# Kernel tuning notes

Measured on AMD Instinct MI355X. Metric: run time of the kernel, lower is better.

Reference implementation:

```python
import jax, jax.numpy as jnp
import numpy as np

C = 16          # in_channels // 4
EXP = 16        # expand_rate
SHIFTS = [1, 3, 5, 7]
BN_EPS = 1e-5

# fixed directional-difference kernels (non-trainable in the torch module)
_tmp1 = np.array([[[-1,0,0],[0,1,0],[0,0,0]],
                  [[0,-1,0],[0,1,0],[0,0,0]],
                  [[0,0,-1],[0,1,0],[0,0,0]],
                  [[0,0,0],[-1,1,0],[0,0,0]]], dtype=np.float32).reshape(4,1,3,3)
_tmp2 = _tmp1[:, :, ::-1, ::-1].copy()
K1 = jnp.asarray(np.tile(np.concatenate([_tmp1, _tmp2], 0), (C,1,1,1)))  # [8C,1,3,3]
K2 = jnp.asarray(np.tile(np.concatenate([_tmp2, _tmp1], 0), (C,1,1,1)))  # [8C,1,3,3]

def conv(x, w, groups=1, dilation=1, bias=None):
    out = jax.lax.conv_general_dilated(
        x, w, window_strides=(1,1), padding='SAME',
        rhs_dilation=(dilation, dilation),
        dimension_numbers=('NCHW','OIHW','NCHW'),
        feature_group_count=groups)
    if bias is not None:
        out = out + bias[None, :, None, None]
    return out

def setup_inputs() -> dict:
    key = jax.random.key(0)
    ks = jax.random.split(key, 20)
    B, Cin, H, W = 4, 64, 256, 256
    inp = {
        'cen': jax.random.normal(ks[0], (B, Cin, H, W), jnp.float32),
        'mas': jax.random.normal(ks[1], (B, 1, H, W), jnp.float32),
        'w_in': jax.random.normal(ks[2], (C, Cin, 1, 1), jnp.float32) * 0.1,
        'b_in': jax.random.normal(ks[3], (C,), jnp.float32) * 0.1,
        'w_c0': jax.random.normal(ks[4], (C, C, 1, 1), jnp.float32) * 0.1,
        'b_c0': jax.random.normal(ks[5], (C,), jnp.float32) * 0.1,
        'w_c1': jax.random.normal(ks[6], (C, C, 3, 3), jnp.float32) * 0.1,
        'b_c1': jax.random.normal(ks[7], (C,), jnp.float32) * 0.1,
        'w_c2': jax.random.normal(ks[8], (C, C, 5, 5), jnp.float32) * 0.05,
        'b_c2': jax.random.normal(ks[9], (C,), jnp.float32) * 0.1,
        'w_c3': jax.random.normal(ks[10], (C, C, 7, 7), jnp.float32) * 0.05,
        'b_c3': jax.random.normal(ks[11], (C,), jnp.float32) * 0.1,
        'scales1': jax.random.normal(ks[12], (4,), jnp.float32) * 0.1,
        'scales2': jax.random.normal(ks[13], (C * EXP, 8, 1, 1), jnp.float32) * 0.1,
        'scales3': jax.random.normal(ks[14], (C, EXP, 1, 1), jnp.float32) * 0.1,
        'w_base': jax.random.normal(ks[15], (C, C, 3, 3), jnp.float32) * 0.1,
        'bn_gamma': jnp.ones((C,), jnp.float32),
        'bn_beta': jnp.zeros((C,), jnp.float32),
        'bn_mean': jnp.zeros((C,), jnp.float32),
        'bn_var': jnp.ones((C,), jnp.float32),
        'w_out': jax.random.normal(ks[16], (1, C, 1, 1), jnp.float32) * 0.1,
        'b_out': jax.random.normal(ks[17], (1,), jnp.float32) * 0.1,
    }
    return inp

def reference(cen, mas, w_in, b_in, w_c0, b_c0, w_c1, b_c1, w_c2, b_c2, w_c3, b_c3,
              scales1, scales2, scales3, w_base, bn_gamma, bn_beta, bn_mean, bn_var,
              w_out, b_out):
    x = conv(cen, w_in, bias=b_in)                      # [B,C,H,W]
    k3 = jax.nn.softmax(scales2, axis=1)                # [8C*2? no: [C*EXP,8,1,1]
    k4 = jax.nn.softmax(scales3, axis=1)                # [C,EXP,1,1]
    conv_ws = [(w_c0, b_c0), (w_c1, b_c1), (w_c2, b_c2), (w_c3, b_c3)]
    outs = []
    for (wc, bc), shift in zip(conv_ws, SHIFTS):
        c = conv(x, wc, bias=bc)                        # [B,C,H,W]
        o1 = conv(c, K1, groups=C, dilation=shift)      # [B,8C,H,W]
        o2 = conv(c, K2, groups=C, dilation=shift)
        o1 = conv(o1, k3, groups=C)                     # [B,C*EXP,H,W]
        o2 = conv(o2, k3, groups=C)
        o = jnp.sort(o1 * o2, axis=2)                   # sort along H
        o = jax.nn.silu(o)
        o = conv(o, k4, groups=C)                       # [B,C,H,W]
        outs.append(o)
    outs = jnp.stack(outs, axis=-1)                     # [B,C,H,W,4]
    outs = jnp.max(outs, axis=-1) + jnp.mean(outs, axis=-1)
    # out_conv = BaseConv(3x3 conv -> BN(eval) -> SiLU) then 1x1 conv to 1 ch
    h = conv(outs, w_base)
    h = (h - bn_mean[None, :, None, None]) * jax.lax.rsqrt(bn_var + BN_EPS)[None, :, None, None]
    h = h * bn_gamma[None, :, None, None] + bn_beta[None, :, None, None]
    h = jax.nn.silu(h)
    h = conv(h, w_out, bias=b_out)
    out_mask = jax.nn.sigmoid(h)                        # [B,1,H,W]
    s = jax.nn.softmax(scales1, axis=-1)
    m = jax.nn.sigmoid(mas)
    return cen * (out_mask * m * s[0] + m * s[1] + s[2] * out_mask + s[3])
```

## Files before the change

### kernel.cpp

```cpp
#include <hip/hip_runtime.h>

#define HW 65536

constexpr int OFF_X    = 0;
constexpr int OFF_CT   = 4194304;
constexpr int OFF_MAX  = 8388608;
constexpr int OFF_SUM  = 12582912;
constexpr int P_K3  = 17039360;
constexpr int P_K3S = P_K3  + 2048;
constexpr int P_K4  = P_K3S + 2048;
constexpr int P_S1  = P_K4  + 256;
constexpr int P_BNS = P_S1  + 4;
constexpr int P_BNB = P_BNS + 16;
constexpr int P_WRI = P_BNB + 16;
constexpr int P_WR0 = P_WRI + 1024;
constexpr int P_WR1 = P_WR0 + 256;
constexpr int P_WR2 = P_WR1 + 2304;
constexpr int P_WR3 = P_WR2 + 6400;
constexpr int P_WRB = P_WR3 + 12544;
constexpr int P_K3U = P_WRB + 2304;
constexpr int P_K3V = P_K3U + 512;

typedef _Float16 hv2 __attribute__((ext_vector_type(2)));

__device__ __forceinline__ int h2i(hv2 v) { return __builtin_bit_cast(int, v); }
__device__ __forceinline__ hv2 i2h(int v) { return __builtin_bit_cast(hv2, v); }

__device__ __forceinline__ hv2 pkrtz(float a, float b) {
  return __builtin_bit_cast(hv2, __builtin_amdgcn_cvt_pkrtz(a, b));
}

__device__ __forceinline__ hv2 pk_fma_n(hv2 a, hv2 b, hv2 c) {
#if __has_builtin(__builtin_elementwise_fma)
  return __builtin_elementwise_fma(a, b, c);
#else
  return a * b + c;
#endif
}

__device__ __forceinline__ hv2 pkmin(hv2 a, hv2 b) {
  hv2 d; asm("v_pk_min_f16 %0, %1, %2" : "=v"(d) : "v"(a), "v"(b)); return d;
}
__device__ __forceinline__ hv2 pkmax(hv2 a, hv2 b) {
  hv2 d; asm("v_pk_max_f16 %0, %1, %2" : "=v"(d) : "v"(a), "v"(b)); return d;
}
__device__ __forceinline__ hv2 pkmul(hv2 a, hv2 b) {
  hv2 d; asm("v_pk_mul_f16 %0, %1, %2" : "=v"(d) : "v"(a), "v"(b)); return d;
}
__device__ __forceinline__ hv2 pkfma(hv2 a, hv2 b, hv2 c) {
  hv2 d; asm("v_pk_fma_f16 %0, %1, %2, %3" : "=v"(d) : "v"(a), "v"(b), "v"(c)); return d;
}

__device__ __forceinline__ hv2 sel32(bool c, hv2 a, hv2 b) {
  return i2h(c ? h2i(a) : h2i(b));
}

template <int LMASK>
__device__ __forceinline__ int lane_xor_i(int x) {
  if constexpr (LMASK < 32) {
    return __builtin_amdgcn_ds_swizzle(x, (LMASK << 10) | 0x1F);
  } else {
    return __shfl_xor(x, LMASK, 64);
  }
}

__device__ __forceinline__ float sigmoid_fast(float x) {
  return __fdividef(1.0f, 1.0f + __expf(-x));
}

__global__ void k_prep(const float* __restrict__ w_in, const float* __restrict__ w_c0,
                       const float* __restrict__ w_c1, const float* __restrict__ w_c2,
                       const float* __restrict__ w_c3, const float* __restrict__ w_base,
                       const float* __restrict__ scales1, const float* __restrict__ scales2,
                       const float* __restrict__ scales3, const float* __restrict__ bn_gamma,
                       const float* __restrict__ bn_beta, const float* __restrict__ bn_mean,
                       const float* __restrict__ bn_var, float* __restrict__ ws) {
  int tid = threadIdx.x;
  {
    const float* srow = scales2 + tid * 8;
    float v[8]; float mx = -1e30f;
    for (int j = 0; j < 8; j++) { v[j] = srow[j]; mx = fmaxf(mx, v[j]); }
    float s = 0.f;
    for (int j = 0; j < 8; j++) { v[j] = __expf(v[j] - mx); s += v[j]; }
    float inv = 1.0f / s;
    for (int j = 0; j < 8; j++) ws[P_K3 + tid * 8 + j] = v[j] * inv;
  }
  if (tid < 16) {
    const float* srow = scales3 + tid * 16;
    float v[16]; float mx = -1e30f;
    for (int e = 0; e < 16; e++) { v[e] = srow[e]; mx = fmaxf(mx, v[e]); }
    float s = 0.f;
    for (int e = 0; e < 16; e++) { v[e] = __expf(v[e] - mx); s += v[e]; }
    float inv = 1.0f / s;
    for (int e = 0; e < 16; e++) ws[P_K4 + tid * 16 + e] = v[e] * inv;
  }
  if (tid == 0) {
    float v[4]; float mx = -1e30f;
    for (int i = 0; i < 4; i++) { v[i] = scales1[i]; mx = fmaxf(mx, v[i]); }
    float s = 0.f;
    for (int i = 0; i < 4; i++) { v[i] = __expf(v[i] - mx); s += v[i]; }
    for (int i = 0; i < 4; i++) ws[P_S1 + i] = v[i] / s;
  }
  if (tid < 16) {
    float rs = rsqrtf(bn_var[tid] + 1e-5f);
    float sc = bn_gamma[tid] * rs;
    ws[P_BNS + tid] = sc;
    ws[P_BNB + tid] = bn_beta[tid] - bn_mean[tid] * sc;
  }
  for (int i = tid; i < 1024; i += 256) { int ci = i >> 4, co = i & 15; ws[P_WRI + i] = w_in[co * 64 + ci]; }
  {
    uint32_t* w0 = (uint32_t*)(ws + P_WR0);
    for (int i = tid; i < 128; i += 256) {
      int cp = i & 7, ci = i >> 3;
      hv2 wv;
      wv.x = (_Float16)w_c0[(2 * cp) * 16 + ci];
      wv.y = (_Float16)w_c0[(2 * cp + 1) * 16 + ci];
      w0[ci * 8 + cp] = __builtin_bit_cast(uint32_t, wv);
    }
    uint32_t* w1 = (uint32_t*)(ws + P_WR1);
    for (int i = tid; i < 1152; i += 256) {
      int cp = i & 7; int r = i >> 3; int kw = r % 3; r /= 3; int kh = r % 3; int ci = r / 3;
      hv2 wv;
      wv.x = (_Float16)w_c1[((2 * cp) * 16 + ci) * 9 + kh * 3 + kw];
      wv.y = (_Float16)w_c1[((2 * cp + 1) * 16 + ci) * 9 + kh * 3 + kw];
      w1[((ci * 3 + kh) * 3 + kw) * 8 + cp] = __builtin_bit_cast(uint32_t, wv);
    }
    uint32_t* w2 = (uint32_t*)(ws + P_WR2);
    for (int i = tid; i < 3200; i += 256) {
      int cp = i & 7; int r = i >> 3; int kw = r % 5; r /= 5; int kh = r % 5; int ci = r / 5;
      hv2 wv;
      wv.x = (_Float16)w_c2[((2 * cp) * 16 + ci) * 25 + kh * 5 + kw];
      wv.y = (_Float16)w_c2[((2 * cp + 1) * 16 + ci) * 25 + kh * 5 + kw];
      w2[((ci * 5 + kh) * 5 + kw) * 8 + cp] = __builtin_bit_cast(uint32_t, wv);
    }
    uint32_t* w3 = (uint32_t*)(ws + P_WR3);
    for (int i = tid; i < 6272; i += 256) {
      int cp = i & 7; int r = i >> 3; int kw = r % 7; r /= 7; int kh = r % 7; int ci = r / 7;
      hv2 wv;
      wv.x = (_Float16)w_c3[((2 * cp) * 16 + ci) * 49 + kh * 7 + kw];
      wv.y = (_Float16)w_c3[((2 * cp + 1) * 16 + ci) * 49 + kh * 7 + kw];
      w3[((ci * 7 + kh) * 7 + kw) * 8 + cp] = __builtin_bit_cast(uint32_t, wv);
    }
  }
  for (int i = tid; i < 2304; i += 256) {
    int co = i & 15; int r = i >> 4; int kh = r % 3; r /= 3; int kw = r % 3; int g = r / 3;
    ws[P_WRB + i] = w_base[((co * 16 + g) * 3 + kh) * 3 + kw];
  }
  __syncthreads();
  uint32_t* k3u = (uint32_t*)(ws + P_K3U);
  uint32_t* k3v = (uint32_t*)(ws + P_K3V);
  for (int i = tid; i < 512; i += 256) {
    int g = i >> 5, p = (i >> 2) & 7, j = i & 3;
    const float* r0 = ws + P_K3 + g * 128 + (2 * p) * 8;
    const float* r1 = ws + P_K3 + g * 128 + (2 * p + 1) * 8;
    hv2 wu, wv;
    wu.x = (_Float16)((r0[j] + r0[j + 4]) * 0.5f);
    wu.y = (_Float16)((r1[j] + r1[j + 4]) * 0.5f);
    wv.x = (_Float16)((r0[j] - r0[j + 4]) * 0.5f);
    wv.y = (_Float16)((r1[j] - r1[j + 4]) * 0.5f);
    k3u[i] = __builtin_bit_cast(uint32_t, wu);
    k3v[i] = __builtin_bit_cast(uint32_t, wv);
  }
}

__global__ __launch_bounds__(256) void k_in(const float* __restrict__ cen,
                                            const float* __restrict__ b_in,
                                            const float* __restrict__ ws,
                                            float* __restrict__ xT) {
  __shared__ float ldst[16 * 16 * 17];
  int tid = threadIdx.x;
  int b = blockIdx.z;
  int hbase = blockIdx.y * 16, wbase = blockIdx.x * 16;
  int ty = tid >> 4, tx = tid & 15;
  const float* wri = ws + P_WRI;
  float acc[16];
#pragma unroll
  for (int co = 0; co < 16; co++) acc[co] = b_in[co];
  const float* cp = cen + b * 64 * HW + (hbase + ty) * 256 + wbase + tx;
#pragma unroll 4
  for (int ci = 0; ci < 64; ci++) {
    float v = cp[ci * HW];
#pragma unroll
    for (int co = 0; co < 16; co++) acc[co] = fmaf(wri[ci * 16 + co], v, acc[co]);
  }
#pragma unroll
  for (int co = 0; co < 16; co++) ldst[(co * 16 + tx) * 17 + ty] = acc[co];
  __syncthreads();
  int wy = tid >> 4, hx = tid & 15;
#pragma unroll
  for (int ci = 0; ci < 16; ci++) {
    xT[((b * 16 + ci) << 16) + (wbase + wy) * 256 + hbase + hx] =
        ldst[(ci * 16 + wy) * 17 + hx];
  }
}

template <int KS, bool SAFE>
__device__ __forceinline__ void conv_body(const float* __restrict__ xb,
                                          const uint32_t* __restrict__ wrh,
                                          int w, int hbase, int lane, hv2 acc[8]) {
  constexpr int P = KS / 2;
#pragma unroll 2
  for (int ci = 0; ci < 16; ci++) {
#pragma unroll
    for (int kw = 0; kw < KS; kw++) {
      const int wc = w + kw - P;
      if (KS > 1 && (unsigned)wc >= 256u) continue;
      const float* col = xb + (ci << 16) + (wc << 8);
      const int hb = hbase + lane - P;
#pragma unroll
      for (int kh = 0; kh < KS; kh++) {
        float tv;
        if constexpr (SAFE) {
          tv = col[hb + kh];
        } else {
          const int h = hb + kh;
          tv = ((unsigned)h < 256u) ? col[h] : 0.0f;
        }
        const hv2 tp = pkrtz(tv, tv);
        const uint32_t* wp = wrh + ((ci * KS + kh) * KS + kw) * 8;
#pragma unroll
        for (int cp = 0; cp < 8; cp++)
          acc[cp] = pk_fma_n(i2h((int)wp[cp]), tp, acc[cp]);
      }
    }
  }
}

template <int KS>
__global__ __launch_bounds__(256) void k_conv(const float* __restrict__ xT,
                                              const float* __restrict__ bias,
                                              const uint32_t* __restrict__ wrh,
                                              float* __restrict__ cT) {
  const int tid = threadIdx.x;
  const int lane = tid & 63;
  const int wv = (blockIdx.x << 2) + (tid >> 6);
  const int hseg = wv & 3;
  const int w = (wv >> 2) & 255;
  const int b = wv >> 10;
  const int hbase = hseg << 6;
  const float* xb = xT + ((b * 16) << 16);

  hv2 acc[8];
#pragma unroll
  for (int cp = 0; cp < 8; cp++) {
    hv2 bv;
    bv.x = (_Float16)bias[2 * cp];
    bv.y = (_Float16)bias[2 * cp + 1];
    acc[cp] = bv;
  }

  if (KS == 1 || (hseg != 0 && hseg != 3)) {
    conv_body<KS, true>(xb, wrh, w, hbase, lane, acc);
  } else {
    conv_body<KS, false>(xb, wrh, w, hbase, lane, acc);
  }

  float* o = cT + ((b * 16) << 16) + (w << 8) + hbase + lane;
#pragma unroll
  for (int cp = 0; cp < 8; cp++) {
    o[(2 * cp) << 16] = (float)acc[cp].x;
    o[(2 * cp + 1) << 16] = (float)acc[cp].y;
  }
}

__device__ __forceinline__ void ce_pair_h(hv2& a, hv2& b, bool up) {
  hv2 lo = pkmin(a, b);
  hv2 hi = pkmax(a, b);
  a = sel32(up, lo, hi);
  b = sel32(up, hi, lo);
}

template <int SIZE, int DIST>
__device__ __forceinline__ void stage_x_h(hv2 v[4], int i0) {
  const bool keepmin = (((i0 & DIST) == 0) == ((i0 & SIZE) == 0));
#pragma unroll
  for (int r = 0; r < 4; r++) {
    hv2 pv = i2h(lane_xor_i<(DIST >> 2)>(h2i(v[r])));
    v[r] = sel32(keepmin, pkmin(v[r], pv), pkmax(v[r], pv));
  }
}

template <int SIZE>
__device__ __forceinline__ void stage_d21_h(hv2 v[4], int i0) {
  bool up = ((i0 & SIZE) == 0);
  ce_pair_h(v[0], v[2], up); ce_pair_h(v[1], v[3], up);
  ce_pair_h(v[0], v[1], up); ce_pair_h(v[2], v[3], up);
}

__device__ __forceinline__ void sort256h(hv2 v[4], int lane) {
  int i0 = lane << 2;
  ce_pair_h(v[0], v[1], true); ce_pair_h(v[2], v[3], false);
  stage_d21_h<4>(v, i0);
  stage_x_h<8, 4>(v, i0); stage_d21_h<8>(v, i0);
  stage_x_h<16, 8>(v, i0); stage_x_h<16, 4>(v, i0); stage_d21_h<16>(v, i0);
  stage_x_h<32, 16>(v, i0); stage_x_h<32, 8>(v, i0); stage_x_h<32, 4>(v, i0); stage_d21_h<32>(v, i0);
  stage_x_h<64, 32>(v, i0); stage_x_h<64, 16>(v, i0); stage_x_h<64, 8>(v, i0); stage_x_h<64, 4>(v, i0); stage_d21_h<64>(v, i0);
  stage_x_h<128, 64>(v, i0); stage_x_h<128, 32>(v, i0); stage_x_h<128, 16>(v, i0); stage_x_h<128, 8>(v, i0); stage_x_h<128, 4>(v, i0); stage_d21_h<128>(v, i0);
  stage_x_h<256, 128>(v, i0); stage_x_h<256, 64>(v, i0); stage_x_h<256, 32>(v, i0); stage_x_h<256, 16>(v, i0); stage_x_h<256, 8>(v, i0); stage_x_h<256, 4>(v, i0); stage_d21_h<256>(v, i0);
}

template <int DIL>
__global__ __launch_bounds__(256) void k_branch(const float* __restrict__ cT,
                                                const float* __restrict__ ws,
                                                float* __restrict__ maxb,
                                                float* __restrict__ sumb,
                                                int initFlag) {
  const int tid = threadIdx.x;
  const int lane = tid & 63;
  const int wid = __builtin_amdgcn_readfirstlane(tid >> 6);
  const int wv = (blockIdx.x << 2) + wid;
  const int w = wv & 255;
  const int g = (wv >> 8) & 15;
  const int b = wv >> 12;
  const float* base = cT + ((b * 16 + g) << 16);

  float vals[3][3][4];
#pragma unroll
  for (int wi = 0; wi < 3; ++wi) {
    const int wc = w + (wi - 1) * DIL;
    const bool wok = ((unsigned)wc < 256u);
    const float* col = base + (wok ? wc : 0) * 256;
#pragma unroll
    for (int si = 0; si < 3; ++si) {
#pragma unroll
      for (int r = 0; r < 4; ++r) {
        const int h = lane + (r << 6) + (si - 1) * DIL;
        const bool ok = wok && ((unsigned)h < 256u);
        vals[wi][si][r] = ok ? col[h] : 0.0f;
      }
    }
  }
  hv2 uh[4][4], vh[4][4];
#pragma unroll
  for (int r = 0; r < 4; ++r) {
    const float c0 = vals[1][1][r];
    float d0 = c0 - vals[0][0][r];
    float d1 = c0 - vals[1][0][r];
    float d2 = c0 - vals[2][0][r];
    float d3 = c0 - vals[0][1][r];
    float d4 = c0 - vals[2][2][r];
    float d5 = c0 - vals[1][2][r];
    float d6 = c0 - vals[0][2][r];
    float d7 = c0 - vals[2][1][r];
    uh[0][r] = pkrtz(d0 + d4, d0 + d4);
    uh[1][r] = pkrtz(d1 + d5, d1 + d5);
    uh[2][r] = pkrtz(d2 + d6, d2 + d6);
    uh[3][r] = pkrtz(d3 + d7, d3 + d7);
    vh[0][r] = pkrtz(d0 - d4, d0 - d4);
    vh[1][r] = pkrtz(d1 - d5, d1 - d5);
    vh[2][r] = pkrtz(d2 - d6, d2 - d6);
    vh[3][r] = pkrtz(d3 - d7, d3 - d7);
  }
  float out[4] = {0.f, 0.f, 0.f, 0.f};
  const uint32_t* k3u = (const uint32_t*)(ws + P_K3U) + g * 32;
  const uint32_t* k3v = (const uint32_t*)(ws + P_K3V) + g * 32;
  const float* k4p = ws + P_K4 + g * 16;
#pragma unroll 1
  for (int p = 0; p < 8; ++p) {
    hv2 t[4];
    hv2 wu[4], wvv[4];
#pragma unroll
    for (int j = 0; j < 4; ++j) {
      wu[j]  = i2h((int)k3u[p * 4 + j]);
      wvv[j] = i2h((int)k3v[p * 4 + j]);
    }
#pragma unroll
    for (int r = 0; r < 4; ++r) {
      hv2 s = pkmul(wu[0], uh[0][r]);
      s = pkfma(wu[1], uh[1][r], s);
      s = pkfma(wu[2], uh[2][r], s);
      s = pkfma(wu[3], uh[3][r], s);
      hv2 d = pkmul(wvv[0], vh[0][r]);
      d = pkfma(wvv[1], vh[1][r], d);
      d = pkfma(wvv[2], vh[2][r], d);
      d = pkfma(wvv[3], vh[3][r], d);
      t[r] = pkmul(s + d, s - d);
    }
    sort256h(t, lane);
    const float k4a = k4p[2 * p], k4b = k4p[2 * p + 1];
#pragma unroll
    for (int r = 0; r < 4; ++r) {
      const float va = (float)t[r].x;
      const float vb = (float)t[r].y;
      out[r] = fmaf(k4a, va * sigmoid_fast(va), out[r]);
      out[r] = fmaf(k4b, vb * sigmoid_fast(vb), out[r]);
    }
  }
  const int obase = (((b * 16 + g) << 8) + w) * 256 + (lane << 2);
  float4 o4 = make_float4(out[0], out[1], out[2], out[3]);
  float4* mp = (float4*)(maxb + obase);
  float4* sp = (float4*)(sumb + obase);
  if (initFlag) {
    *mp = o4;
    *sp = o4;
  } else {
    float4 m = *mp;
    m.x = fmaxf(m.x, o4.x); m.y = fmaxf(m.y, o4.y);
    m.z = fmaxf(m.z, o4.z); m.w = fmaxf(m.w, o4.w);
    *mp = m;
    float4 s = *sp;
    s.x += o4.x; s.y += o4.y; s.z += o4.z; s.w += o4.w;
    *sp = s;
  }
}

__global__ __launch_bounds__(256) void k_tail(const float* __restrict__ maxb,
                                              const float* __restrict__ sumb,
                                              const float* __restrict__ ws,
                                              const float* __restrict__ cen,
                                              const float* __restrict__ mas,
                                              const float* __restrict__ w_out,
                                              const float* __restrict__ b_out,
                                              float* __restrict__ out) {
  __shared__ float lds[16 * 18 * 18];
  __shared__ float ldsf[256];
  int tid = threadIdx.x;
  int b = blockIdx.z;
  int wbase = blockIdx.x * 16, hbase = blockIdx.y * 16;
  const float* mb = maxb + (b * 16) * HW;
  const float* sb = sumb + (b * 16) * HW;
  for (int i = tid; i < 16 * 18 * 18; i += 256) {
    int g = i / 324; int r = i % 324; int xx = r / 18, yy = r % 18;
    int wq = wbase + xx - 1, hq = hbase + yy - 1;
    float v = 0.0f;
    if (wq >= 0 && wq < 256 && hq >= 0 && hq < 256) {
      int idx = g * HW + wq * 256 + hq;
      v = mb[idx] + 0.25f * sb[idx];
    }
    lds[i] = v;
  }
  __syncthreads();
  int xw = tid >> 4, yh = tid & 15;
  float acc[16] = {0.f, 0.f, 0.f, 0.f, 0.f, 0.f, 0.f, 0.f,
                   0.f, 0.f, 0.f, 0.f, 0.f, 0.f, 0.f, 0.f};
  for (int g = 0; g < 16; g++) {
#pragma unroll
    for (int kw = 0; kw < 3; kw++) {
#pragma unroll
      for (int kh = 0; kh < 3; kh++) {
        float v = lds[g * 324 + (xw + kw) * 18 + (yh + kh)];
        const float* wp = ws + P_WRB + ((g * 3 + kw) * 3 + kh) * 16;
#pragma unroll
        for (int co = 0; co < 16; co++) acc[co] = fmaf(wp[co], v, acc[co]);
      }
    }
  }
  float mo = b_out[0];
#pragma unroll
  for (int co = 0; co < 16; co++) {
    float z = acc[co] * ws[P_BNS + co] + ws[P_BNB + co];
    float sl = z * sigmoid_fast(z);
    mo = fmaf(w_out[co], sl, mo);
  }
  float mk = sigmoid_fast(mo);
  ldsf[yh * 16 + xw] = mk;
  __syncthreads();
  {
    int yy = tid >> 4, xx = tid & 15;
    float mkv = ldsf[yy * 16 + xx];
    float m = sigmoid_fast(mas[b * HW + (hbase + yy) * 256 + wbase + xx]);
    float s0 = ws[P_S1], s1 = ws[P_S1 + 1], s2 = ws[P_S1 + 2], s3 = ws[P_S1 + 3];
    float f = mkv * m * s0 + m * s1 + s2 * mkv + s3;
    ldsf[yy * 16 + xx] = f;
  }
  __syncthreads();
  const float* cb = cen + b * 64 * HW;
  float* ob = out + b * 64 * HW;
#pragma unroll 4
  for (int it = 0; it < 16; ++it) {
    int flat = it * 256 + tid;
    int ci = flat >> 6;
    int rr = flat & 63;
    int yy = rr >> 2, wq = rr & 3;
    const float* fr = &ldsf[yy * 16 + wq * 4];
    float4 f4 = make_float4(fr[0], fr[1], fr[2], fr[3]);
    int addr = ci * HW + (hbase + yy) * 256 + wbase + wq * 4;
    const float4 c4 = *(const float4*)(cb + addr);
    float4 o4;
    o4.x = c4.x * f4.x; o4.y = c4.y * f4.y; o4.z = c4.z * f4.z; o4.w = c4.w * f4.w;
    *(float4*)(ob + addr) = o4;
  }
}

extern "C" void kernel_launch(void* const* d_in, const int* in_sizes, int n_in,
                              void* d_out, int out_size, void* d_ws, size_t ws_size,
                              hipStream_t stream) {
  (void)in_sizes; (void)n_in; (void)out_size; (void)ws_size;
  const float* cen = (const float*)d_in[0];
  const float* mas = (const float*)d_in[1];
  const float* w_in = (const float*)d_in[2];
  const float* b_in = (const float*)d_in[3];
  const float* w_c0 = (const float*)d_in[4];
  const float* b_c0 = (const float*)d_in[5];
  const float* w_c1 = (const float*)d_in[6];
  const float* b_c1 = (const float*)d_in[7];
  const float* w_c2 = (const float*)d_in[8];
  const float* b_c2 = (const float*)d_in[9];
  const float* w_c3 = (const float*)d_in[10];
  const float* b_c3 = (const float*)d_in[11];
  const float* scales1 = (const float*)d_in[12];
  const float* scales2 = (const float*)d_in[13];
  const float* scales3 = (const float*)d_in[14];
  const float* w_base = (const float*)d_in[15];
  const float* bn_gamma = (const float*)d_in[16];
  const float* bn_beta = (const float*)d_in[17];
  const float* bn_mean = (const float*)d_in[18];
  const float* bn_var = (const float*)d_in[19];
  const float* w_out = (const float*)d_in[20];
  const float* b_out = (const float*)d_in[21];
  float* ws = (float*)d_ws;
  float* out = (float*)d_out;

  float* xT = ws + OFF_X;
  float* cT = ws + OFF_CT;
  float* maxb = ws + OFF_MAX;
  float* sumb = ws + OFF_SUM;

  k_prep<<<1, 256, 0, stream>>>(w_in, w_c0, w_c1, w_c2, w_c3, w_base, scales1, scales2,
                                scales3, bn_gamma, bn_beta, bn_mean, bn_var, ws);
  k_in<<<dim3(16, 16, 4), 256, 0, stream>>>(cen, b_in, ws, xT);

  k_conv<1><<<1024, 256, 0, stream>>>(xT, b_c0, (const uint32_t*)(ws + P_WR0), cT);
  k_branch<1><<<4096, 256, 0, stream>>>(cT, ws, maxb, sumb, 1);
  k_conv<3><<<1024, 256, 0, stream>>>(xT, b_c1, (const uint32_t*)(ws + P_WR1), cT);
  k_branch<3><<<4096, 256, 0, stream>>>(cT, ws, maxb, sumb, 0);
  k_conv<5><<<1024, 256, 0, stream>>>(xT, b_c2, (const uint32_t*)(ws + P_WR2), cT);
  k_branch<5><<<4096, 256, 0, stream>>>(cT, ws, maxb, sumb, 0);
  k_conv<7><<<1024, 256, 0, stream>>>(xT, b_c3, (const uint32_t*)(ws + P_WR3), cT);
  k_branch<7><<<4096, 256, 0, stream>>>(cT, ws, maxb, sumb, 0);

  k_tail<<<dim3(16, 16, 4), 256, 0, stream>>>(maxb, sumb, ws, cen, mas, w_out, b_out, out);
}
```

Before: 865.0 us.

## Fuse four dilation branches into one kernel with in-register max/mean reduction

Stores all four conv outputs in separate workspace slices, then runs a single branch kernel that processes every dilation per wave and reduces max plus 0.25·sum in registers. This writes one combined buffer instead of repeatedly reading and writing max and sum buffers, and cuts the launch count. The parameter region is moved to the front of the workspace, and a fallback path keeps the old per-branch sequence when the workspace is too small. The fused kernel does four times the work per wave, which lengthens its runtime and may raise register pressure.

```diff
diff --git a/kernel.cpp b/kernel.cpp
--- a/kernel.cpp
+++ b/kernel.cpp
@@ -2,24 +2,22 @@
 
 #define HW 65536
 
-constexpr int OFF_X    = 0;
-constexpr int OFF_CT   = 4194304;
-constexpr int OFF_MAX  = 8388608;
-constexpr int OFF_SUM  = 12582912;
-constexpr int P_K3  = 17039360;
-constexpr int P_K3S = P_K3  + 2048;
-constexpr int P_K4  = P_K3S + 2048;
-constexpr int P_S1  = P_K4  + 256;
-constexpr int P_BNS = P_S1  + 4;
-constexpr int P_BNB = P_BNS + 16;
-constexpr int P_WRI = P_BNB + 16;
-constexpr int P_WR0 = P_WRI + 1024;
-constexpr int P_WR1 = P_WR0 + 256;
-constexpr int P_WR2 = P_WR1 + 2304;
-constexpr int P_WR3 = P_WR2 + 6400;
-constexpr int P_WRB = P_WR3 + 12544;
-constexpr int P_K3U = P_WRB + 2304;
-constexpr int P_K3V = P_K3U + 512;
+constexpr int P_K3  = 0;
+constexpr int P_K4  = 2048;
+constexpr int P_S1  = 2304;
+constexpr int P_BNS = 2308;
+constexpr int P_BNB = 2324;
+constexpr int P_WRI = 2340;
+constexpr int P_WR0 = 3364;
+constexpr int P_WR1 = 3492;
+constexpr int P_WR2 = 4644;
+constexpr int P_WR3 = 7844;
+constexpr int P_WRB = 14116;
+constexpr int P_K3U = 16420;
+constexpr int P_K3V = 16932;
+constexpr int OFF_X  = 32768;
+constexpr int OFF_CT = 32768 + 4194304;
+constexpr int CTSZ   = 4194304;
 
 typedef _Float16 hv2 __attribute__((ext_vector_type(2)));
 
@@ -300,20 +298,9 @@
 }
 
 template <int DIL>
-__global__ __launch_bounds__(256) void k_branch(const float* __restrict__ cT,
-                                                const float* __restrict__ ws,
-                                                float* __restrict__ maxb,
-                                                float* __restrict__ sumb,
-                                                int initFlag) {
-  const int tid = threadIdx.x;
-  const int lane = tid & 63;
-  const int wid = __builtin_amdgcn_readfirstlane(tid >> 6);
-  const int wv = (blockIdx.x << 2) + wid;
-  const int w = wv & 255;
-  const int g = (wv >> 8) & 15;
-  const int b = wv >> 12;
-  const float* base = cT + ((b * 16 + g) << 16);
-
+__device__ __forceinline__ void branch_one(const float* __restrict__ base,
+                                           const float* __restrict__ ws,
+                                           int g, int w, int lane, float out[4]) {
   float vals[3][3][4];
 #pragma unroll
   for (int wi = 0; wi < 3; ++wi) {
@@ -351,7 +338,7 @@
     vh[2][r] = pkrtz(d2 - d6, d2 - d6);
     vh[3][r] = pkrtz(d3 - d7, d3 - d7);
   }
-  float out[4] = {0.f, 0.f, 0.f, 0.f};
+  out[0] = out[1] = out[2] = out[3] = 0.f;
   const uint32_t* k3u = (const uint32_t*)(ws + P_K3U) + g * 32;
   const uint32_t* k3v = (const uint32_t*)(ws + P_K3V) + g * 32;
   const float* k4p = ws + P_K4 + g * 16;
@@ -386,6 +373,60 @@
       out[r] = fmaf(k4b, vb * sigmoid_fast(vb), out[r]);
     }
   }
+}
+
+__global__ __launch_bounds__(256) void k_branch4(const float* __restrict__ cT,
+                                                 const float* __restrict__ ws,
+                                                 float* __restrict__ comb) {
+  const int tid = threadIdx.x;
+  const int lane = tid & 63;
+  const int wid = __builtin_amdgcn_readfirstlane(tid >> 6);
+  const int wv = (blockIdx.x << 2) + wid;
+  const int w = wv & 255;
+  const int g = (wv >> 8) & 15;
+  const int b = wv >> 12;
+  const int boff = (b * 16 + g) << 16;
+
+  float out[4], mx[4], sm[4];
+  branch_one<1>(cT + 0 * CTSZ + boff, ws, g, w, lane, out);
+#pragma unroll
+  for (int r = 0; r < 4; ++r) { mx[r] = out[r]; sm[r] = out[r]; }
+  branch_one<3>(cT + 1 * CTSZ + boff, ws, g, w, lane, out);
+#pragma unroll
+  for (int r = 0; r < 4; ++r) { mx[r] = fmaxf(mx[r], out[r]); sm[r] += out[r]; }
+  branch_one<5>(cT + 2 * CTSZ + boff, ws, g, w, lane, out);
+#pragma unroll
+  for (int r = 0; r < 4; ++r) { mx[r] = fmaxf(mx[r], out[r]); sm[r] += out[r]; }
+  branch_one<7>(cT + 3 * CTSZ + boff, ws, g, w, lane, out);
+#pragma unroll
+  for (int r = 0; r < 4; ++r) { mx[r] = fmaxf(mx[r], out[r]); sm[r] += out[r]; }
+
+  const int obase = (((b * 16 + g) << 8) + w) * 256 + (lane << 2);
+  float4 o4;
+  o4.x = fmaf(0.25f, sm[0], mx[0]);
+  o4.y = fmaf(0.25f, sm[1], mx[1]);
+  o4.z = fmaf(0.25f, sm[2], mx[2]);
+  o4.w = fmaf(0.25f, sm[3], mx[3]);
+  *(float4*)(comb + obase) = o4;
+}
+
+template <int DIL>
+__global__ __launch_bounds__(256) void k_branch(const float* __restrict__ cT,
+                                                const float* __restrict__ ws,
+                                                float* __restrict__ maxb,
+                                                float* __restrict__ sumb,
+                                                int initFlag) {
+  const int tid = threadIdx.x;
+  const int lane = tid & 63;
+  const int wid = __builtin_amdgcn_readfirstlane(tid >> 6);
+  const int wv = (blockIdx.x << 2) + wid;
+  const int w = wv & 255;
+  const int g = (wv >> 8) & 15;
+  const int b = wv >> 12;
+
+  float out[4];
+  branch_one<DIL>(cT + ((b * 16 + g) << 16), ws, g, w, lane, out);
+
   const int obase = (((b * 16 + g) << 8) + w) * 256 + (lane << 2);
   float4 o4 = make_float4(out[0], out[1], out[2], out[3]);
   float4* mp = (float4*)(maxb + obase);
@@ -404,28 +445,30 @@
   }
 }
 
-__global__ __launch_bounds__(256) void k_tail(const float* __restrict__ maxb,
-                                              const float* __restrict__ sumb,
+__global__ __launch_bounds__(256) void k_tail(const float* __restrict__ a,
+                                              const float* __restrict__ sb,
                                               const float* __restrict__ ws,
                                               const float* __restrict__ cen,
                                               const float* __restrict__ mas,
                                               const float* __restrict__ w_out,
                                               const float* __restrict__ b_out,
-                                              float* __restrict__ out) {
+                                              float* __restrict__ out,
+                                              int combMode) {
   __shared__ float lds[16 * 18 * 18];
   __shared__ float ldsf[256];
   int tid = threadIdx.x;
   int b = blockIdx.z;
   int wbase = blockIdx.x * 16, hbase = blockIdx.y * 16;
-  const float* mb = maxb + (b * 16) * HW;
-  const float* sb = sumb + (b * 16) * HW;
+  const float* mb = a + (b * 16) * HW;
+  const float* sbb = sb + (b * 16) * HW;
   for (int i = tid; i < 16 * 18 * 18; i += 256) {
     int g = i / 324; int r = i % 324; int xx = r / 18, yy = r % 18;
     int wq = wbase + xx - 1, hq = hbase + yy - 1;
     float v = 0.0f;
     if (wq >= 0 && wq < 256 && hq >= 0 && hq < 256) {
       int idx = g * HW + wq * 256 + hq;
-      v = mb[idx] + 0.25f * sb[idx];
+      v = mb[idx];
+      if (!combMode) v += 0.25f * sbb[idx];
     }
     lds[i] = v;
   }
@@ -485,7 +528,7 @@
 extern "C" void kernel_launch(void* const* d_in, const int* in_sizes, int n_in,
                               void* d_out, int out_size, void* d_ws, size_t ws_size,
                               hipStream_t stream) {
-  (void)in_sizes; (void)n_in; (void)out_size; (void)ws_size;
+  (void)in_sizes; (void)n_in; (void)out_size;
   const float* cen = (const float*)d_in[0];
   const float* mas = (const float*)d_in[1];
   const float* w_in = (const float*)d_in[2];
@@ -513,21 +556,33 @@
 
   float* xT = ws + OFF_X;
   float* cT = ws + OFF_CT;
-  float* maxb = ws + OFF_MAX;
-  float* sumb = ws + OFF_SUM;
+
+  const size_t needFused = (size_t)(OFF_CT + 4 * CTSZ) * 4;
+  const bool fused = ws_size >= needFused;
 
   k_prep<<<1, 256, 0, stream>>>(w_in, w_c0, w_c1, w_c2, w_c3, w_base, scales1, scales2,
                                 scales3, bn_gamma, bn_beta, bn_mean, bn_var, ws);
   k_in<<<dim3(16, 16, 4), 256, 0, stream>>>(cen, b_in, ws, xT);
 
-  k_conv<1><<<1024, 256, 0, stream>>>(xT, b_c0, (const uint32_t*)(ws + P_WR0), cT);
-  k_branch<1><<<4096, 256, 0, stream>>>(cT, ws, maxb, sumb, 1);
-  k_conv<3><<<1024, 256, 0, stream>>>(xT, b_c1, (const uint32_t*)(ws + P_WR1), cT);
-  k_branch<3><<<4096, 256, 0, stream>>>(cT, ws, maxb, sumb, 0);
-  k_conv<5><<<1024, 256, 0, stream>>>(xT, b_c2, (const uint32_t*)(ws + P_WR2), cT);
-  k_branch<5><<<4096, 256, 0, stream>>>(cT, ws, maxb, sumb, 0);
-  k_conv<7><<<1024, 256, 0, stream>>>(xT, b_c3, (const uint32_t*)(ws + P_WR3), cT);
-  k_branch<7><<<4096, 256, 0, stream>>>(cT, ws, maxb, sumb, 0);
-
-  k_tail<<<dim3(16, 16, 4), 256, 0, stream>>>(maxb, sumb, ws, cen, mas, w_out, b_out, out);
-}
+  if (fused) {
+    k_conv<1><<<1024, 256, 0, stream>>>(xT, b_c0, (const uint32_t*)(ws + P_WR0), cT + 0 * CTSZ);
+    k_conv<3><<<1024, 256, 0, stream>>>(xT, b_c1, (const uint32_t*)(ws + P_WR1), cT + 1 * CTSZ);
+    k_conv<5><<<1024, 256, 0, stream>>>(xT, b_c2, (const uint32_t*)(ws + P_WR2), cT + 2 * CTSZ);
+    k_conv<7><<<1024, 256, 0, stream>>>(xT, b_c3, (const uint32_t*)(ws + P_WR3), cT + 3 * CTSZ);
+    float* comb = xT;
+    k_branch4<<<4096, 256, 0, stream>>>(cT, ws, comb);
+    k_tail<<<dim3(16, 16, 4), 256, 0, stream>>>(comb, comb, ws, cen, mas, w_out, b_out, out, 1);
+  } else {
+    float* maxb = cT + CTSZ;
+    float* sumb = cT + 2 * CTSZ;
+    k_conv<1><<<1024, 256, 0, stream>>>(xT, b_c0, (const uint32_t*)(ws + P_WR0), cT);
+    k_branch<1><<<4096, 256, 0, stream>>>(cT, ws, maxb, sumb, 1);
+    k_conv<3><<<1024, 256, 0, stream>>>(xT, b_c1, (const uint32_t*)(ws + P_WR1), cT);
+    k_branch<3><<<4096, 256, 0, stream>>>(cT, ws, maxb, sumb, 0);
+    k_conv<5><<<1024, 256, 0, stream>>>(xT, b_c2, (const uint32_t*)(ws + P_WR2), cT);
+    k_branch<5><<<4096, 256, 0, stream>>>(cT, ws, maxb, sumb, 0);
+    k_conv<7><<<1024, 256, 0, stream>>>(xT, b_c3, (const uint32_t*)(ws + P_WR3), cT);
+    k_branch<7><<<4096, 256, 0, stream>>>(cT, ws, maxb, sumb, 0);
+    k_tail<<<dim3(16, 16, 4), 256, 0, stream>>>(maxb, sumb, ws, cen, mas, w_out, b_out, out, 0);
+  }
+}
```

Result: slower. 882.3 us, median of 2 (+2.0%).
